# Performance work log

Measured on AMD Instinct MI355X. Metric: run time of the kernel, lower is better.

Reference implementation:

```python
import jax, jax.numpy as jnp
import numpy as np

R = 3                 # search_radius
S2 = (2 * R + 1) ** 2  # 49 correlation channels
VIS_PIXEL_SCALE = 0.1  # arcsec / pixel


def _interp_tokens(tokens, sh, sw, dh, dw):
    # tokens [B, N, D] on (sh, sw) grid -> (dh, dw) grid
    B, N, D = tokens.shape
    x = jnp.transpose(tokens, (0, 2, 1)).reshape(B, D, sh, sw)
    if (sh, sw) != (dh, dw):
        # torch F.interpolate bilinear align_corners=False == jax half-pixel bilinear
        x = jax.image.resize(x, (B, D, dh, dw), method='bilinear')
    return x  # [B, D, dh, dw]


def _l2norm(x, eps=1e-12):
    n = jnp.sqrt(jnp.sum(x * x, axis=1, keepdims=True))
    return x / jnp.maximum(n, eps)


def _corr_volume(q, ref):
    # q, ref: [B, D, H, W]; local cosine-similarity volume [B, S2, H, W]
    q = _l2norm(q)
    ref = _l2norm(ref)
    B, D, H, W = q.shape
    refp = jnp.pad(ref, ((0, 0), (0, 0), (R, R), (R, R)), mode='edge')  # replicate pad
    slices = [
        jnp.sum(q * jax.lax.dynamic_slice(refp, (0, 0, R + dy, R + dx), (B, D, H, W)), axis=1)
        for dy in range(-R, R + 1) for dx in range(-R, R + 1)
    ]
    return jnp.stack(slices, axis=1)


def _conv5(x, w, b):
    y = jax.lax.conv_general_dilated(x, w, (1, 1), 'SAME',
                                     dimension_numbers=('NCHW', 'OIHW', 'NCHW'))
    return y + b[None, :, None, None]


def _refine_net(x, w0, b0, w1, b1, w2, b2):
    h = jax.nn.gelu(_conv5(x, w0, b0), approximate=False)
    h = jax.nn.gelu(_conv5(h, w1, b1), approximate=False)
    return _conv5(h, w2, b2)


def setup_inputs() -> dict:
    key = jax.random.key(0)
    ks = jax.random.split(key, 8)
    B, D = 4, 256
    rubin_tokens = jax.random.normal(ks[0], (B, 64 * 64, D), dtype=jnp.float32)
    vis_tokens = jax.random.normal(ks[1], (B, 128 * 128, D), dtype=jnp.float32)
    in_ch = 2 + S2 + 1  # 52
    hid = 32
    def kaiming(k, shape):
        fan_in = shape[1] * shape[2] * shape[3]
        return jax.random.normal(k, shape, dtype=jnp.float32) / np.sqrt(fan_in)
    w0 = kaiming(ks[2], (hid, in_ch, 5, 5)); b0 = jnp.zeros((hid,), jnp.float32)
    w1 = kaiming(ks[3], (hid, hid, 5, 5));   b1 = jnp.zeros((hid,), jnp.float32)
    w2 = kaiming(ks[4], (2, hid, 5, 5));     b2 = jnp.zeros((2,), jnp.float32)
    log_temp = jnp.asarray(np.log(0.1), dtype=jnp.float32)
    return {
        'rubin_tokens': rubin_tokens, 'vis_tokens': vis_tokens,
        'w0': w0, 'b0': b0, 'w1': w1, 'b1': b1, 'w2': w2, 'b2': b2,
        'log_temp': log_temp,
        'rubin_h': 64, 'rubin_w': 64, 'vis_h': 128, 'vis_w': 128,
        'img_h': 2048, 'img_w': 2048,
    }


def reference(rubin_tokens, vis_tokens, w0, b0, w1, b1, w2, b2, log_temp,
              rubin_h, rubin_w, vis_h, vis_w, img_h, img_w):
    Hc, Wc = max(rubin_h, vis_h), max(rubin_w, vis_w)
    q = _interp_tokens(rubin_tokens, rubin_h, rubin_w, Hc, Wc)  # [B,D,Hc,Wc]
    k = _interp_tokens(vis_tokens, vis_h, vis_w, Hc, Wc)
    corr = _corr_volume(q, k)  # [B,S2,Hc,Wc]

    # soft-argmax over the (2R+1)^2 neighborhood
    coords = jnp.arange(-R, R + 1, dtype=corr.dtype)
    cy, cx = jnp.meshgrid(coords, coords, indexing='ij')
    cy = cy.reshape(1, S2, 1, 1)
    cx = cx.reshape(1, S2, 1, 1)
    temp = jnp.exp(log_temp)
    weights = jax.nn.softmax(corr / temp, axis=1)
    dy = jnp.sum(weights * cy, axis=1, keepdims=True)
    dx = jnp.sum(weights * cx, axis=1, keepdims=True)
    confidence = jnp.max(weights, axis=1, keepdims=True)
    raw_offsets = jnp.concatenate([dy, dx], axis=1)  # [B,2,Hc,Wc]

    x = jnp.concatenate([raw_offsets, corr, confidence], axis=1)  # [B,52,Hc,Wc]
    residual = _refine_net(x, w0, b0, w1, b1, w2, b2)
    refined = raw_offsets + residual

    sky_per_token_y = img_h * VIS_PIXEL_SCALE / Hc
    sky_per_token_x = img_w * VIS_PIXEL_SCALE / Wc
    dra = refined[:, 1:2] * sky_per_token_x
    ddec = refined[:, 0:1] * sky_per_token_y
    # [B,5,Hc,Wc]: dra, ddec, raw_dy, raw_dx, confidence
    return jnp.concatenate([dra, ddec, dy, dx, confidence], axis=1)
```

## Files before the change

kernel.cpp:

```cpp
#include <hip/hip_runtime.h>
#include <math.h>

#define Hh 128
#define Ww 128
#define Dd 256
#define Bb 4
#define HW (Hh*Ww)
#define NPIX (Bb*HW)
#define WP 132

typedef __attribute__((ext_vector_type(8))) short s16x8;
typedef __attribute__((ext_vector_type(4))) float f32x4;

__device__ __forceinline__ float wsum(float v) {
#pragma unroll
    for (int o = 32; o; o >>= 1) v += __shfl_xor(v, o, 64);
    return v;
}

__device__ __forceinline__ unsigned short f2bf(float f) {
    unsigned u = __float_as_uint(f);
    u += 0x7FFF + ((u >> 16) & 1);
    return (unsigned short)(u >> 16);
}

__device__ __forceinline__ float gelu_exact(float v) {
    return 0.5f * v * (1.0f + erff(v * 0.70710678118654752f));
}

#define ZGRAN 1115136
__global__ __launch_bounds__(256) void setup_fill(const float* __restrict__ w0,
                                                  const float* __restrict__ w1,
                                                  const float* __restrict__ w2,
                                                  unsigned short* __restrict__ wb0,
                                                  unsigned short* __restrict__ wb1,
                                                  unsigned short* __restrict__ wb2,
                                                  uint4* __restrict__ zbase) {
    int t = blockIdx.x * 256 + threadIdx.x;
    if (t < ZGRAN) {
        zbase[t] = (uint4){0, 0, 0, 0};
        return;
    }
    int u = t - ZGRAN;
    if (u < 51200) {
        int tap = u >> 11; int r = u & 2047; int n = r >> 6; int k = r & 63;
        wb0[u] = (k < 52) ? f2bf(w0[n * 1300 + k * 25 + tap]) : (unsigned short)0;
    } else if (u < 76800) {
        int v = u - 51200; int tap = v >> 10; int r = v & 1023; int n = r >> 5; int k = r & 31;
        wb1[v] = f2bf(w1[n * 800 + k * 25 + tap]);
    } else if (u < 89600) {
        int v = u - 76800; int tap = v >> 9; int r = v & 511; int n = r >> 5; int k = r & 31;
        wb2[v] = (n < 2) ? f2bf(w2[n * 800 + k * 25 + tap]) : (unsigned short)0;
    }
}

__global__ __launch_bounds__(256) void norm_fused(const float* __restrict__ vis,
                                                  const float* __restrict__ rub,
                                                  unsigned short* __restrict__ kn,
                                                  unsigned short* __restrict__ qn) {
    int wid = threadIdx.x >> 6, lane = threadIdx.x & 63;
    int blk = blockIdx.x;
    if (blk < 16384) {
        int pix = blk * 4 + wid;
        const float4 v = *(const float4*)(vis + (size_t)pix * Dd + lane * 4);
        float ss = wsum(v.x * v.x + v.y * v.y + v.z * v.z + v.w * v.w);
        float inv = 1.0f / fmaxf(sqrtf(ss), 1e-12f);
        ushort4 o;
        o.x = f2bf(v.x * inv); o.y = f2bf(v.y * inv);
        o.z = f2bf(v.z * inv); o.w = f2bf(v.w * inv);
        *(ushort4*)(kn + (size_t)pix * Dd + lane * 4) = o;
    } else {
        int pix = (blk - 16384) * 4 + wid;
        int b = pix >> 14; int yx = pix & 16383; int y = yx >> 7; int x = yx & 127;
        float sy = 0.5f * y - 0.25f;
        float sx = 0.5f * x - 0.25f;
        int y0 = (int)floorf(sy); float fy = sy - (float)y0;
        int x0 = (int)floorf(sx); float fx = sx - (float)x0;
        int y0c = max(y0, 0), y1c = min(y0 + 1, 63);
        int x0c = max(x0, 0), x1c = min(x0 + 1, 63);
        const float* base = rub + (size_t)b * 4096 * Dd;
        const float4 v00 = *(const float4*)(base + (size_t)(y0c * 64 + x0c) * Dd + lane * 4);
        const float4 v01 = *(const float4*)(base + (size_t)(y0c * 64 + x1c) * Dd + lane * 4);
        const float4 v10 = *(const float4*)(base + (size_t)(y1c * 64 + x0c) * Dd + lane * 4);
        const float4 v11 = *(const float4*)(base + (size_t)(y1c * 64 + x1c) * Dd + lane * 4);
        float w00 = (1.f - fy) * (1.f - fx), w01 = (1.f - fy) * fx;
        float w10 = fy * (1.f - fx), w11 = fy * fx;
        float4 v;
        v.x = w00 * v00.x + w01 * v01.x + w10 * v10.x + w11 * v11.x;
        v.y = w00 * v00.y + w01 * v01.y + w10 * v10.y + w11 * v11.y;
        v.z = w00 * v00.z + w01 * v01.z + w10 * v10.z + w11 * v11.z;
        v.w = w00 * v00.w + w01 * v01.w + w10 * v10.w + w11 * v11.w;
        float ss = wsum(v.x * v.x + v.y * v.y + v.z * v.z + v.w * v.w);
        float inv = 1.0f / fmaxf(sqrtf(ss), 1e-12f);
        ushort4 o;
        o.x = f2bf(v.x * inv); o.y = f2bf(v.y * inv);
        o.z = f2bf(v.z * inv); o.w = f2bf(v.w * inv);
        *(ushort4*)(qn + (size_t)pix * Dd + lane * 4) = o;
    }
}

__global__ __launch_bounds__(1024) void corr_block(const unsigned short* __restrict__ qn,
                                                   const unsigned short* __restrict__ kn,
                                                   const float* __restrict__ log_temp,
                                                   unsigned short* __restrict__ xb,
                                                   float* __restrict__ out) {
    __shared__ char smem[484 * 5 * 16];
    int tid = threadIdx.x;
    int wid = tid >> 6, lane = tid & 63, l15 = lane & 15, quad = lane >> 4;
    int blk = blockIdx.x;
    int b = blk >> 6, rem = blk & 63;
    int y0 = ((rem >> 3) & 7) << 4, x0 = (rem & 7) << 4;
    int y = y0 + wid;

    const unsigned short* src0; int dst0;
    const unsigned short* src1 = nullptr; int dst1 = 0;
    bool hav1;
    {
        int g = tid;
        int px = g >> 2, sub = g & 3;
        int ry = px / 22, rx = px - ry * 22;
        int yy = min(max(y0 - 3 + ry, 0), 127);
        int xx = min(max(x0 - 3 + rx, 0), 127);
        src0 = kn + ((size_t)(b << 14) + yy * 128 + xx) * 256 + sub * 8;
        dst0 = (px * 5 + sub) * 16;
        g = 1024 + tid;
        hav1 = (g < 1936);
        int gc = hav1 ? g : 1935;
        px = gc >> 2; sub = gc & 3;
        ry = px / 22; rx = px - ry * 22;
        yy = min(max(y0 - 3 + ry, 0), 127);
        xx = min(max(x0 - 3 + rx, 0), 127);
        src1 = kn + ((size_t)(b << 14) + yy * 128 + xx) * 256 + sub * 8;
        dst1 = (px * 5 + sub) * 16;
    }
    int lpixoff[10];
#pragma unroll
    for (int f = 0; f < 10; f++) {
        int p = min(f * 16 + l15, 153);
        int pr = p / 22, pc = p - pr * 22;
        lpixoff[f] = (((wid + pr) * 22 + pc) * 5 + quad) * 16;
    }
    const unsigned short* aptr = qn + ((size_t)(b << 14) + y * 128 + x0 + l15) * 256 + quad * 8;

    f32x4 acc[10];
#pragma unroll
    for (int f = 0; f < 10; f++) acc[f] = (f32x4){0.f, 0.f, 0.f, 0.f};

    uint4 v0 = *(const uint4*)src0;
    uint4 v1 = *(const uint4*)src1;
    s16x8 an = *(const s16x8*)aptr;
    for (int c = 0; c < 8; c++) {
        uint4 w0v = v0, w1v = v1;
        s16x8 a = an;
        if (c < 7) {
            v0 = *(const uint4*)(src0 + (c + 1) * 32);
            v1 = *(const uint4*)(src1 + (c + 1) * 32);
            an = *(const s16x8*)(aptr + (c + 1) * 32);
        }
        __syncthreads();
        *(uint4*)(smem + dst0) = w0v;
        if (hav1) *(uint4*)(smem + dst1) = w1v;
        __syncthreads();
#pragma unroll
        for (int f = 0; f < 10; f++) {
            s16x8 bf = *(const s16x8*)(smem + lpixoff[f]);
            acc[f] = __builtin_amdgcn_mfma_f32_16x16x32_bf16(a, bf, acc[f], 0, 0, 0);
        }
    }

    float inv_temp = expf(-log_temp[0]);
    float vmax[4] = {-1e30f, -1e30f, -1e30f, -1e30f};
#pragma unroll
    for (int f = 0; f < 10; f++) {
        int n = f * 16 + l15;
        if (n <= 153) {
            int dy = n / 22 - 3;
            int rx = n - (dy + 3) * 22;
#pragma unroll
            for (int i = 0; i < 4; i++) {
                int m = quad * 4 + i;
                int dx = rx - m - 3;
                if ((unsigned)(dx + 3) <= 6u) vmax[i] = fmaxf(vmax[i], acc[f][i]);
            }
        }
    }
#pragma unroll
    for (int o = 1; o <= 8; o <<= 1) {
#pragma unroll
        for (int i = 0; i < 4; i++) vmax[i] = fmaxf(vmax[i], __shfl_xor(vmax[i], o, 64));
    }
    float se[4] = {0, 0, 0, 0}, sey[4] = {0, 0, 0, 0}, sex[4] = {0, 0, 0, 0}, emax[4] = {0, 0, 0, 0};
    unsigned short* xrow = xb + ((size_t)(b * WP + y + 2) * WP + x0 + 2) * 64;
#pragma unroll
    for (int f = 0; f < 10; f++) {
        int n = f * 16 + l15;
        if (n <= 153) {
            int dy = n / 22 - 3;
            int rx = n - (dy + 3) * 22;
#pragma unroll
            for (int i = 0; i < 4; i++) {
                int m = quad * 4 + i;
                int dx = rx - m - 3;
                if ((unsigned)(dx + 3) <= 6u) {
                    float v = acc[f][i];
                    float e = expf((v - vmax[i]) * inv_temp);
                    se[i] += e;
                    sey[i] += e * (float)dy;
                    sex[i] += e * (float)dx;
                    emax[i] = fmaxf(emax[i], e);
                    xrow[(size_t)m * 64 + 2 + (dy + 3) * 7 + (dx + 3)] = f2bf(v);
                }
            }
        }
    }
#pragma unroll
    for (int o = 1; o <= 8; o <<= 1) {
#pragma unroll
        for (int i = 0; i < 4; i++) {
            se[i] += __shfl_xor(se[i], o, 64);
            sey[i] += __shfl_xor(sey[i], o, 64);
            sex[i] += __shfl_xor(sex[i], o, 64);
            emax[i] = fmaxf(emax[i], __shfl_xor(emax[i], o, 64));
        }
    }
    if (l15 == 0) {
#pragma unroll
        for (int i = 0; i < 4; i++) {
            int m = quad * 4 + i;
            float inv_se = 1.0f / se[i];
            float dyv = sey[i] * inv_se, dxv = sex[i] * inv_se, conf = emax[i] * inv_se;
            unsigned short* xp = xrow + (size_t)m * 64;
            xp[0] = f2bf(dyv); xp[1] = f2bf(dxv); xp[51] = f2bf(conf);
            float* op = out + (size_t)b * 5 * HW + y * 128 + x0 + m;
            op[2 * HW] = dyv; op[3 * HW] = dxv; op[4 * HW] = conf;
        }
    }
}

template <int ICP, int OC, bool GELU>
__global__ __launch_bounds__(256) void conv_lds(const unsigned short* __restrict__ in,
                                                const unsigned short* __restrict__ wb,
                                                const float* __restrict__ bias,
                                                unsigned short* __restrict__ outp) {
    constexpr int AG = ICP / 8;
    constexpr int ASTR = AG + 1;
    constexpr int WSTR = AG + 1;
    constexpr int NF = OC / 16;
    constexpr int KS = ICP / 32;
    constexpr int ABYTES = 132 * ASTR * 16;
    constexpr int WBYTES = 5 * OC * WSTR * 16;
    __shared__ char smem[ABYTES + WBYTES];
    uint4* aLDS = (uint4*)smem;
    uint4* wLDS = (uint4*)(smem + ABYTES);

    int tid = threadIdx.x;
    int wid = tid >> 6, lane = tid & 63, l15 = lane & 15, quad = lane >> 4;
    int blk = blockIdx.x;
    int b = blk >> 7, y = blk & 127;

    f32x4 acc0[NF], acc1[NF];
#pragma unroll
    for (int g = 0; g < NF; g++) { acc0[g] = (f32x4){0,0,0,0}; acc1[g] = (f32x4){0,0,0,0}; }

    for (int ky = 0; ky < 5; ky++) {
        __syncthreads();
        const uint4* asrc = (const uint4*)(in + ((size_t)(b * WP + y + ky) * WP) * ICP);
        constexpr int AGR = 132 * AG;
#pragma unroll
        for (int i = 0; i < (AGR + 255) / 256; i++) {
            int g = i * 256 + tid;
            if (g < AGR) {
                int px = g / AG, sub = g % AG;
                aLDS[px * ASTR + sub] = asrc[g];
            }
        }
        const uint4* wsrc = (const uint4*)(wb + (size_t)(ky * 5) * OC * ICP);
        constexpr int WGR = 5 * OC * AG;
#pragma unroll
        for (int i = 0; i < (WGR + 255) / 256; i++) {
            int g = i * 256 + tid;
            if (g < WGR) {
                int nl = g / AG, sub = g % AG;
                wLDS[nl * WSTR + sub] = wsrc[g];
            }
        }
        __syncthreads();
#pragma unroll
        for (int kx = 0; kx < 5; kx++) {
#pragma unroll
            for (int ks = 0; ks < KS; ks++) {
                int abyte = ((32 * wid + l15 + kx) * ASTR + ks * 4 + quad) * 16;
                s16x8 a0 = *(const s16x8*)(smem + abyte);
                s16x8 a1 = *(const s16x8*)(smem + abyte + 16 * ASTR * 16);
#pragma unroll
                for (int g = 0; g < NF; g++) {
                    int wbyte = ABYTES + ((kx * OC + g * 16 + l15) * WSTR + ks * 4 + quad) * 16;
                    s16x8 bf = *(const s16x8*)(smem + wbyte);
                    acc0[g] = __builtin_amdgcn_mfma_f32_16x16x32_bf16(a0, bf, acc0[g], 0, 0, 0);
                    acc1[g] = __builtin_amdgcn_mfma_f32_16x16x32_bf16(a1, bf, acc1[g], 0, 0, 0);
                }
            }
        }
    }
    size_t orow = ((size_t)(b * WP + y + 2) * WP + 2) * OC;
#pragma unroll
    for (int g = 0; g < NF; g++) {
        float bv = bias[g * 16 + l15];
#pragma unroll
        for (int r = 0; r < 4; r++) {
            int px0 = 32 * wid + quad * 4 + r;
            float v0 = acc0[g][r] + bv;
            float v1 = acc1[g][r] + bv;
            if (GELU) { v0 = gelu_exact(v0); v1 = gelu_exact(v1); }
            outp[orow + (size_t)px0 * OC + g * 16 + l15] = f2bf(v0);
            outp[orow + (size_t)(px0 + 16) * OC + g * 16 + l15] = f2bf(v1);
        }
    }
}

__global__ __launch_bounds__(256) void conv_final_lds(const unsigned short* __restrict__ in,
                                                      const unsigned short* __restrict__ wb,
                                                      const float* __restrict__ bias,
                                                      float* __restrict__ out) {
    constexpr int ICP = 32, OC = 16;
    constexpr int AG = 4, ASTR = 5, WSTR = 5;
    constexpr int ABYTES = 132 * ASTR * 16;
    constexpr int WBYTES = 5 * OC * WSTR * 16;
    __shared__ char smem[ABYTES + WBYTES];
    __shared__ float cl[4][32][2];
    uint4* aLDS = (uint4*)smem;
    uint4* wLDS = (uint4*)(smem + ABYTES);

    int tid = threadIdx.x;
    int wid = tid >> 6, lane = tid & 63, l15 = lane & 15, quad = lane >> 4;
    int blk = blockIdx.x;
    int b = blk >> 7, y = blk & 127;

    f32x4 acc0 = (f32x4){0,0,0,0}, acc1 = (f32x4){0,0,0,0};

    for (int ky = 0; ky < 5; ky++) {
        __syncthreads();
        const uint4* asrc = (const uint4*)(in + ((size_t)(b * WP + y + ky) * WP) * ICP);
        constexpr int AGR = 132 * AG;
#pragma unroll
        for (int i = 0; i < 3; i++) {
            int g = i * 256 + tid;
            if (g < AGR) {
                int px = g / AG, sub = g % AG;
                aLDS[px * ASTR + sub] = asrc[g];
            }
        }
        const uint4* wsrc = (const uint4*)(wb + (size_t)(ky * 5) * OC * ICP);
        constexpr int WGR = 5 * OC * AG;
#pragma unroll
        for (int i = 0; i < 2; i++) {
            int g = i * 256 + tid;
            if (g < WGR) {
                int nl = g / AG, sub = g % AG;
                wLDS[nl * WSTR + sub] = wsrc[g];
            }
        }
        __syncthreads();
#pragma unroll
        for (int kx = 0; kx < 5; kx++) {
            int abyte = ((32 * wid + l15 + kx) * ASTR + quad) * 16;
            s16x8 a0 = *(const s16x8*)(smem + abyte);
            s16x8 a1 = *(const s16x8*)(smem + abyte + 16 * ASTR * 16);
            int wbyte = ABYTES + ((kx * OC + l15) * WSTR + quad) * 16;
            s16x8 bf = *(const s16x8*)(smem + wbyte);
            acc0 = __builtin_amdgcn_mfma_f32_16x16x32_bf16(a0, bf, acc0, 0, 0, 0);
            acc1 = __builtin_amdgcn_mfma_f32_16x16x32_bf16(a1, bf, acc1, 0, 0, 0);
        }
    }
    if (l15 < 2) {
        float bv = bias[l15];
#pragma unroll
        for (int r = 0; r < 4; r++) {
            cl[wid][quad * 4 + r][l15] = acc0[r] + bv;
            cl[wid][16 + quad * 4 + r][l15] = acc1[r] + bv;
        }
    }
    __syncthreads();
    if (lane < 32) {
        int px = lane;
        size_t p5 = (size_t)b * 5 * HW + y * Ww + 32 * wid + px;
        float a0 = cl[wid][px][0], a1 = cl[wid][px][1];
        float dy = out[p5 + 2 * HW], dx = out[p5 + 3 * HW];
        out[p5] = (dx + a1) * 1.6f;
        out[p5 + HW] = (dy + a0) * 1.6f;
    }
}

extern "C" void kernel_launch(void* const* d_in, const int* in_sizes, int n_in,
                              void* d_out, int out_size, void* d_ws, size_t ws_size,
                              hipStream_t stream) {
    const float* rub = (const float*)d_in[0];
    const float* vis = (const float*)d_in[1];
    const float* w0 = (const float*)d_in[2];
    const float* b0 = (const float*)d_in[3];
    const float* w1 = (const float*)d_in[4];
    const float* b1 = (const float*)d_in[5];
    const float* w2 = (const float*)d_in[6];
    const float* b2 = (const float*)d_in[7];
    const float* log_temp = (const float*)d_in[8];
    float* out = (float*)d_out;

    char* ws = (char*)d_ws;
    size_t off = 0;
    const size_t PADPIX = (size_t)Bb * WP * WP;
    unsigned short* kn = (unsigned short*)(ws + off); off += (size_t)NPIX * Dd * 2;
    unsigned short* qn = (unsigned short*)(ws + off); off += (size_t)NPIX * Dd * 2;
    unsigned short* xbp = (unsigned short*)(ws + off); off += PADPIX * 64 * 2;
    unsigned short* h1p = (unsigned short*)(ws + off); off += PADPIX * 32 * 2;
    unsigned short* h2p = (unsigned short*)(ws + off); off += PADPIX * 32 * 2;
    unsigned short* wb0 = (unsigned short*)(ws + off); off += 51200 * 2;
    unsigned short* wb1 = (unsigned short*)(ws + off); off += 25600 * 2;
    unsigned short* wb2 = (unsigned short*)(ws + off); off += 12800 * 2;

    setup_fill<<<4706, 256, 0, stream>>>(w0, w1, w2, wb0, wb1, wb2, (uint4*)xbp);
    norm_fused<<<32768, 256, 0, stream>>>(vis, rub, kn, qn);
    corr_block<<<256, 1024, 0, stream>>>(qn, kn, log_temp, xbp, out);
    conv_lds<64, 32, true><<<512, 256, 0, stream>>>(xbp, wb0, b0, h1p);
    conv_lds<32, 32, true><<<512, 256, 0, stream>>>(h1p, wb1, b1, h2p);
    conv_final_lds<<<512, 256, 0, stream>>>(h2p, wb2, b2, out);
}
```

Measured before the change: 230.9 us.

## Tile convs as 16x16 spatial blocks with halo in LDS; 16-lane norm groups

The three 5x5 conv kernels change from one output row per block, which reloads five input rows per row, to 16x16 output tiles with a 20x20 halo loaded into LDS once per channel slice. This cuts redundant global and LDS traffic for the activation inputs. The normalization kernel now uses 16 lanes per pixel with four float4 loads each, a 16-lane shuffle reduction and rsq, giving more work per thread. Costs are 1024-thread blocks, only 256 blocks for the conv stages, and more syncs per channel slice, which could reduce occupancy and overlap.

```diff
diff --git a/kernel.cpp b/kernel.cpp
--- a/kernel.cpp
+++ b/kernel.cpp
@@ -11,12 +11,6 @@
 
 typedef __attribute__((ext_vector_type(8))) short s16x8;
 typedef __attribute__((ext_vector_type(4))) float f32x4;
-
-__device__ __forceinline__ float wsum(float v) {
-#pragma unroll
-    for (int o = 32; o; o >>= 1) v += __shfl_xor(v, o, 64);
-    return v;
-}
 
 __device__ __forceinline__ unsigned short f2bf(float f) {
     unsigned u = __float_as_uint(f);
@@ -58,19 +52,32 @@
                                                   const float* __restrict__ rub,
                                                   unsigned short* __restrict__ kn,
                                                   unsigned short* __restrict__ qn) {
-    int wid = threadIdx.x >> 6, lane = threadIdx.x & 63;
+    int tid = threadIdx.x;
+    int g16 = tid >> 4, l = tid & 15;
     int blk = blockIdx.x;
-    if (blk < 16384) {
-        int pix = blk * 4 + wid;
-        const float4 v = *(const float4*)(vis + (size_t)pix * Dd + lane * 4);
-        float ss = wsum(v.x * v.x + v.y * v.y + v.z * v.z + v.w * v.w);
-        float inv = 1.0f / fmaxf(sqrtf(ss), 1e-12f);
-        ushort4 o;
-        o.x = f2bf(v.x * inv); o.y = f2bf(v.y * inv);
-        o.z = f2bf(v.z * inv); o.w = f2bf(v.w * inv);
-        *(ushort4*)(kn + (size_t)pix * Dd + lane * 4) = o;
+    if (blk < 4096) {
+        int pix = blk * 16 + g16;
+        const float* base = vis + (size_t)pix * Dd + l * 4;
+        float4 v[4];
+#pragma unroll
+        for (int i = 0; i < 4; i++) v[i] = *(const float4*)(base + i * 64);
+        float ss = 0.f;
+#pragma unroll
+        for (int i = 0; i < 4; i++)
+            ss += v[i].x * v[i].x + v[i].y * v[i].y + v[i].z * v[i].z + v[i].w * v[i].w;
+#pragma unroll
+        for (int o = 1; o <= 8; o <<= 1) ss += __shfl_xor(ss, o, 64);
+        float inv = __builtin_amdgcn_rsqf(fmaxf(ss, 1e-24f));
+        unsigned short* op = kn + (size_t)pix * Dd + l * 4;
+#pragma unroll
+        for (int i = 0; i < 4; i++) {
+            ushort4 o4;
+            o4.x = f2bf(v[i].x * inv); o4.y = f2bf(v[i].y * inv);
+            o4.z = f2bf(v[i].z * inv); o4.w = f2bf(v[i].w * inv);
+            *(ushort4*)(op + i * 64) = o4;
+        }
     } else {
-        int pix = (blk - 16384) * 4 + wid;
+        int pix = (blk - 4096) * 16 + g16;
         int b = pix >> 14; int yx = pix & 16383; int y = yx >> 7; int x = yx & 127;
         float sy = 0.5f * y - 0.25f;
         float sx = 0.5f * x - 0.25f;
@@ -78,24 +85,40 @@
         int x0 = (int)floorf(sx); float fx = sx - (float)x0;
         int y0c = max(y0, 0), y1c = min(y0 + 1, 63);
         int x0c = max(x0, 0), x1c = min(x0 + 1, 63);
-        const float* base = rub + (size_t)b * 4096 * Dd;
-        const float4 v00 = *(const float4*)(base + (size_t)(y0c * 64 + x0c) * Dd + lane * 4);
-        const float4 v01 = *(const float4*)(base + (size_t)(y0c * 64 + x1c) * Dd + lane * 4);
-        const float4 v10 = *(const float4*)(base + (size_t)(y1c * 64 + x0c) * Dd + lane * 4);
-        const float4 v11 = *(const float4*)(base + (size_t)(y1c * 64 + x1c) * Dd + lane * 4);
+        const float* base = rub + (size_t)b * 4096 * Dd + l * 4;
+        const float* p00 = base + (size_t)(y0c * 64 + x0c) * Dd;
+        const float* p01 = base + (size_t)(y0c * 64 + x1c) * Dd;
+        const float* p10 = base + (size_t)(y1c * 64 + x0c) * Dd;
+        const float* p11 = base + (size_t)(y1c * 64 + x1c) * Dd;
         float w00 = (1.f - fy) * (1.f - fx), w01 = (1.f - fy) * fx;
         float w10 = fy * (1.f - fx), w11 = fy * fx;
-        float4 v;
-        v.x = w00 * v00.x + w01 * v01.x + w10 * v10.x + w11 * v11.x;
-        v.y = w00 * v00.y + w01 * v01.y + w10 * v10.y + w11 * v11.y;
-        v.z = w00 * v00.z + w01 * v01.z + w10 * v10.z + w11 * v11.z;
-        v.w = w00 * v00.w + w01 * v01.w + w10 * v10.w + w11 * v11.w;
-        float ss = wsum(v.x * v.x + v.y * v.y + v.z * v.z + v.w * v.w);
-        float inv = 1.0f / fmaxf(sqrtf(ss), 1e-12f);
-        ushort4 o;
-        o.x = f2bf(v.x * inv); o.y = f2bf(v.y * inv);
-        o.z = f2bf(v.z * inv); o.w = f2bf(v.w * inv);
-        *(ushort4*)(qn + (size_t)pix * Dd + lane * 4) = o;
+        float4 bv[4];
+        float ss = 0.f;
+#pragma unroll
+        for (int i = 0; i < 4; i++) {
+            float4 a = *(const float4*)(p00 + i * 64);
+            float4 b1 = *(const float4*)(p01 + i * 64);
+            float4 c = *(const float4*)(p10 + i * 64);
+            float4 d = *(const float4*)(p11 + i * 64);
+            float4 v;
+            v.x = w00 * a.x + w01 * b1.x + w10 * c.x + w11 * d.x;
+            v.y = w00 * a.y + w01 * b1.y + w10 * c.y + w11 * d.y;
+            v.z = w00 * a.z + w01 * b1.z + w10 * c.z + w11 * d.z;
+            v.w = w00 * a.w + w01 * b1.w + w10 * c.w + w11 * d.w;
+            bv[i] = v;
+            ss += v.x * v.x + v.y * v.y + v.z * v.z + v.w * v.w;
+        }
+#pragma unroll
+        for (int o = 1; o <= 8; o <<= 1) ss += __shfl_xor(ss, o, 64);
+        float inv = __builtin_amdgcn_rsqf(fmaxf(ss, 1e-24f));
+        unsigned short* op = qn + (size_t)pix * Dd + l * 4;
+#pragma unroll
+        for (int i = 0; i < 4; i++) {
+            ushort4 o4;
+            o4.x = f2bf(bv[i].x * inv); o4.y = f2bf(bv[i].y * inv);
+            o4.z = f2bf(bv[i].z * inv); o4.w = f2bf(bv[i].w * inv);
+            *(ushort4*)(op + i * 64) = o4;
+        }
     }
 }
 
@@ -237,157 +260,140 @@
     }
 }
 
-template <int ICP, int OC, bool GELU>
-__global__ __launch_bounds__(256) void conv_lds(const unsigned short* __restrict__ in,
-                                                const unsigned short* __restrict__ wb,
-                                                const float* __restrict__ bias,
-                                                unsigned short* __restrict__ outp) {
-    constexpr int AG = ICP / 8;
-    constexpr int ASTR = AG + 1;
-    constexpr int WSTR = AG + 1;
+template <int KS, int OC, bool GELU>
+__global__ __launch_bounds__(1024) void conv_tile(const unsigned short* __restrict__ in,
+                                                  const unsigned short* __restrict__ wb,
+                                                  const float* __restrict__ bias,
+                                                  unsigned short* __restrict__ outp) {
+    constexpr int ICP = KS * 32;
     constexpr int NF = OC / 16;
-    constexpr int KS = ICP / 32;
-    constexpr int ABYTES = 132 * ASTR * 16;
-    constexpr int WBYTES = 5 * OC * WSTR * 16;
+    constexpr int ABYTES = 400 * 5 * 16;
+    constexpr int WBYTES = 5 * OC * 5 * 16;
     __shared__ char smem[ABYTES + WBYTES];
-    uint4* aLDS = (uint4*)smem;
-    uint4* wLDS = (uint4*)(smem + ABYTES);
-
     int tid = threadIdx.x;
-    int wid = tid >> 6, lane = tid & 63, l15 = lane & 15, quad = lane >> 4;
+    int wv = tid >> 6, lane = tid & 63, l15 = lane & 15, quad = lane >> 4;
     int blk = blockIdx.x;
-    int b = blk >> 7, y = blk & 127;
-
-    f32x4 acc0[NF], acc1[NF];
-#pragma unroll
-    for (int g = 0; g < NF; g++) { acc0[g] = (f32x4){0,0,0,0}; acc1[g] = (f32x4){0,0,0,0}; }
-
-    for (int ky = 0; ky < 5; ky++) {
+    int b = blk >> 6, ty = (blk >> 3) & 7, tx = blk & 7;
+    int y0 = ty * 16, x0 = tx * 16;
+
+    f32x4 acc[NF];
+#pragma unroll
+    for (int g = 0; g < NF; g++) acc[g] = (f32x4){0.f, 0.f, 0.f, 0.f};
+
+    for (int ks = 0; ks < KS; ks++) {
         __syncthreads();
-        const uint4* asrc = (const uint4*)(in + ((size_t)(b * WP + y + ky) * WP) * ICP);
-        constexpr int AGR = 132 * AG;
-#pragma unroll
-        for (int i = 0; i < (AGR + 255) / 256; i++) {
-            int g = i * 256 + tid;
-            if (g < AGR) {
-                int px = g / AG, sub = g % AG;
-                aLDS[px * ASTR + sub] = asrc[g];
-            }
-        }
-        const uint4* wsrc = (const uint4*)(wb + (size_t)(ky * 5) * OC * ICP);
-        constexpr int WGR = 5 * OC * AG;
-#pragma unroll
-        for (int i = 0; i < (WGR + 255) / 256; i++) {
-            int g = i * 256 + tid;
-            if (g < WGR) {
-                int nl = g / AG, sub = g % AG;
-                wLDS[nl * WSTR + sub] = wsrc[g];
-            }
-        }
-        __syncthreads();
-#pragma unroll
-        for (int kx = 0; kx < 5; kx++) {
-#pragma unroll
-            for (int ks = 0; ks < KS; ks++) {
-                int abyte = ((32 * wid + l15 + kx) * ASTR + ks * 4 + quad) * 16;
-                s16x8 a0 = *(const s16x8*)(smem + abyte);
-                s16x8 a1 = *(const s16x8*)(smem + abyte + 16 * ASTR * 16);
+#pragma unroll
+        for (int i = 0; i < 2; i++) {
+            int g = i * 1024 + tid;
+            if (g < 1600) {
+                int px = g >> 2, sub = g & 3;
+                int r = px / 20, c = px - r * 20;
+                *(uint4*)(smem + (px * 5 + sub) * 16) =
+                    *(const uint4*)(in + ((size_t)(b * WP + y0 + r) * WP + x0 + c) * ICP + ks * 32 + sub * 8);
+            }
+        }
+        for (int ky = 0; ky < 5; ky++) {
+            if (ky > 0) __syncthreads();
+            constexpr int WGR = 5 * OC * 4;
+#pragma unroll
+            for (int i = 0; i < (WGR + 1023) / 1024; i++) {
+                int g = i * 1024 + tid;
+                if (g < WGR) {
+                    int nl = g >> 2, sub = g & 3;
+                    *(uint4*)(smem + ABYTES + (nl * 5 + sub) * 16) =
+                        *(const uint4*)(wb + ((size_t)(ky * 5 * OC) + nl) * ICP + ks * 32 + sub * 8);
+                }
+            }
+            __syncthreads();
+#pragma unroll
+            for (int kx = 0; kx < 5; kx++) {
+                int abyte = (((wv + ky) * 20 + l15 + kx) * 5 + quad) * 16;
+                s16x8 a = *(const s16x8*)(smem + abyte);
 #pragma unroll
                 for (int g = 0; g < NF; g++) {
-                    int wbyte = ABYTES + ((kx * OC + g * 16 + l15) * WSTR + ks * 4 + quad) * 16;
+                    int wbyte = ABYTES + ((kx * OC + g * 16 + l15) * 5 + quad) * 16;
                     s16x8 bf = *(const s16x8*)(smem + wbyte);
-                    acc0[g] = __builtin_amdgcn_mfma_f32_16x16x32_bf16(a0, bf, acc0[g], 0, 0, 0);
-                    acc1[g] = __builtin_amdgcn_mfma_f32_16x16x32_bf16(a1, bf, acc1[g], 0, 0, 0);
+                    acc[g] = __builtin_amdgcn_mfma_f32_16x16x32_bf16(a, bf, acc[g], 0, 0, 0);
                 }
             }
         }
     }
-    size_t orow = ((size_t)(b * WP + y + 2) * WP + 2) * OC;
+    size_t orow = ((size_t)(b * WP + y0 + wv + 2) * WP + x0 + 2) * OC;
 #pragma unroll
     for (int g = 0; g < NF; g++) {
         float bv = bias[g * 16 + l15];
 #pragma unroll
         for (int r = 0; r < 4; r++) {
-            int px0 = 32 * wid + quad * 4 + r;
-            float v0 = acc0[g][r] + bv;
-            float v1 = acc1[g][r] + bv;
-            if (GELU) { v0 = gelu_exact(v0); v1 = gelu_exact(v1); }
-            outp[orow + (size_t)px0 * OC + g * 16 + l15] = f2bf(v0);
-            outp[orow + (size_t)(px0 + 16) * OC + g * 16 + l15] = f2bf(v1);
-        }
-    }
-}
-
-__global__ __launch_bounds__(256) void conv_final_lds(const unsigned short* __restrict__ in,
-                                                      const unsigned short* __restrict__ wb,
-                                                      const float* __restrict__ bias,
-                                                      float* __restrict__ out) {
+            int m = quad * 4 + r;
+            float v = acc[g][r] + bv;
+            if (GELU) v = gelu_exact(v);
+            outp[orow + (size_t)m * OC + g * 16 + l15] = f2bf(v);
+        }
+    }
+}
+
+__global__ __launch_bounds__(1024) void conv_final_tile(const unsigned short* __restrict__ in,
+                                                        const unsigned short* __restrict__ wb,
+                                                        const float* __restrict__ bias,
+                                                        float* __restrict__ out) {
     constexpr int ICP = 32, OC = 16;
-    constexpr int AG = 4, ASTR = 5, WSTR = 5;
-    constexpr int ABYTES = 132 * ASTR * 16;
-    constexpr int WBYTES = 5 * OC * WSTR * 16;
+    constexpr int ABYTES = 400 * 5 * 16;
+    constexpr int WBYTES = 5 * OC * 5 * 16;
     __shared__ char smem[ABYTES + WBYTES];
-    __shared__ float cl[4][32][2];
-    uint4* aLDS = (uint4*)smem;
-    uint4* wLDS = (uint4*)(smem + ABYTES);
-
     int tid = threadIdx.x;
-    int wid = tid >> 6, lane = tid & 63, l15 = lane & 15, quad = lane >> 4;
+    int wv = tid >> 6, lane = tid & 63, l15 = lane & 15, quad = lane >> 4;
     int blk = blockIdx.x;
-    int b = blk >> 7, y = blk & 127;
-
-    f32x4 acc0 = (f32x4){0,0,0,0}, acc1 = (f32x4){0,0,0,0};
-
+    int b = blk >> 6, ty = (blk >> 3) & 7, tx = blk & 7;
+    int y0 = ty * 16, x0 = tx * 16;
+
+    f32x4 acc = (f32x4){0.f, 0.f, 0.f, 0.f};
+    __syncthreads();
+#pragma unroll
+    for (int i = 0; i < 2; i++) {
+        int g = i * 1024 + tid;
+        if (g < 1600) {
+            int px = g >> 2, sub = g & 3;
+            int r = px / 20, c = px - r * 20;
+            *(uint4*)(smem + (px * 5 + sub) * 16) =
+                *(const uint4*)(in + ((size_t)(b * WP + y0 + r) * WP + x0 + c) * ICP + sub * 8);
+        }
+    }
     for (int ky = 0; ky < 5; ky++) {
+        if (ky > 0) __syncthreads();
+        constexpr int WGR = 5 * OC * 4;
+        {
+            int g = tid;
+            if (g < WGR) {
+                int nl = g >> 2, sub = g & 3;
+                *(uint4*)(smem + ABYTES + (nl * 5 + sub) * 16) =
+                    *(const uint4*)(wb + ((size_t)(ky * 5 * OC) + nl) * ICP + sub * 8);
+            }
+        }
         __syncthreads();
-        const uint4* asrc = (const uint4*)(in + ((size_t)(b * WP + y + ky) * WP) * ICP);
-        constexpr int AGR = 132 * AG;
-#pragma unroll
-        for (int i = 0; i < 3; i++) {
-            int g = i * 256 + tid;
-            if (g < AGR) {
-                int px = g / AG, sub = g % AG;
-                aLDS[px * ASTR + sub] = asrc[g];
-            }
-        }
-        const uint4* wsrc = (const uint4*)(wb + (size_t)(ky * 5) * OC * ICP);
-        constexpr int WGR = 5 * OC * AG;
-#pragma unroll
-        for (int i = 0; i < 2; i++) {
-            int g = i * 256 + tid;
-            if (g < WGR) {
-                int nl = g / AG, sub = g % AG;
-                wLDS[nl * WSTR + sub] = wsrc[g];
-            }
-        }
-        __syncthreads();
 #pragma unroll
         for (int kx = 0; kx < 5; kx++) {
-            int abyte = ((32 * wid + l15 + kx) * ASTR + quad) * 16;
-            s16x8 a0 = *(const s16x8*)(smem + abyte);
-            s16x8 a1 = *(const s16x8*)(smem + abyte + 16 * ASTR * 16);
-            int wbyte = ABYTES + ((kx * OC + l15) * WSTR + quad) * 16;
+            int abyte = (((wv + ky) * 20 + l15 + kx) * 5 + quad) * 16;
+            s16x8 a = *(const s16x8*)(smem + abyte);
+            int wbyte = ABYTES + ((kx * OC + l15) * 5 + quad) * 16;
             s16x8 bf = *(const s16x8*)(smem + wbyte);
-            acc0 = __builtin_amdgcn_mfma_f32_16x16x32_bf16(a0, bf, acc0, 0, 0, 0);
-            acc1 = __builtin_amdgcn_mfma_f32_16x16x32_bf16(a1, bf, acc1, 0, 0, 0);
+            acc = __builtin_amdgcn_mfma_f32_16x16x32_bf16(a, bf, acc, 0, 0, 0);
         }
     }
     if (l15 < 2) {
         float bv = bias[l15];
 #pragma unroll
         for (int r = 0; r < 4; r++) {
-            cl[wid][quad * 4 + r][l15] = acc0[r] + bv;
-            cl[wid][16 + quad * 4 + r][l15] = acc1[r] + bv;
-        }
-    }
-    __syncthreads();
-    if (lane < 32) {
-        int px = lane;
-        size_t p5 = (size_t)b * 5 * HW + y * Ww + 32 * wid + px;
-        float a0 = cl[wid][px][0], a1 = cl[wid][px][1];
-        float dy = out[p5 + 2 * HW], dx = out[p5 + 3 * HW];
-        out[p5] = (dx + a1) * 1.6f;
-        out[p5 + HW] = (dy + a0) * 1.6f;
+            int m = quad * 4 + r;
+            size_t p5 = (size_t)b * 5 * HW + (y0 + wv) * Ww + x0 + m;
+            float a = acc[r] + bv;
+            if (l15 == 0) {
+                float dyv = out[p5 + 2 * HW];
+                out[p5 + HW] = (dyv + a) * 1.6f;
+            } else {
+                float dxv = out[p5 + 3 * HW];
+                out[p5] = (dxv + a) * 1.6f;
+            }
+        }
     }
 }
 
@@ -418,9 +424,9 @@
     unsigned short* wb2 = (unsigned short*)(ws + off); off += 12800 * 2;
 
     setup_fill<<<4706, 256, 0, stream>>>(w0, w1, w2, wb0, wb1, wb2, (uint4*)xbp);
-    norm_fused<<<32768, 256, 0, stream>>>(vis, rub, kn, qn);
+    norm_fused<<<8192, 256, 0, stream>>>(vis, rub, kn, qn);
     corr_block<<<256, 1024, 0, stream>>>(qn, kn, log_temp, xbp, out);
-    conv_lds<64, 32, true><<<512, 256, 0, stream>>>(xbp, wb0, b0, h1p);
-    conv_lds<32, 32, true><<<512, 256, 0, stream>>>(h1p, wb1, b1, h2p);
-    conv_final_lds<<<512, 256, 0, stream>>>(h2p, wb2, b2, out);
-}
+    conv_tile<2, 32, true><<<256, 1024, 0, stream>>>(xbp, wb0, b0, h1p);
+    conv_tile<1, 32, true><<<256, 1024, 0, stream>>>(h1p, wb1, b1, h2p);
+    conv_final_tile<<<256, 1024, 0, stream>>>(h2p, wb2, b2, out);
+}
```

New measurement: 214.4 us. 7.1% less time.
